# Performance work log

Hardware: AMD Instinct MI355X
Metric: run time of the kernel (lower is better)

The kernel has to match this reference:

```python
import jax, jax.numpy as jnp
import numpy as np

E = 1_000_000
C_IN = 11
H = 64
N_LAYERS = 4
LN_EPS = 1e-5


def setup_inputs() -> dict:
    key = jax.random.key(0)
    ks = jax.random.split(key, 12)
    x = jax.random.normal(ks[0], (E, C_IN), dtype=jnp.float32)
    neighbors = jax.random.randint(ks[1], (E, 4), 0, E)
    s0 = 1.0 / np.sqrt(5 * C_IN)
    s1 = 1.0 / np.sqrt(5 * H)
    w0 = jax.random.uniform(ks[2], (5 * C_IN, H), jnp.float32, -s0, s0)
    b0 = jax.random.uniform(ks[3], (H,), jnp.float32, -s0, s0)
    w_rest = jax.random.uniform(ks[4], (N_LAYERS - 1, 5 * H, H), jnp.float32, -s1, s1)
    b_rest = jax.random.uniform(ks[5], (N_LAYERS - 1, H), jnp.float32, -s1, s1)
    ln_g = jnp.ones((N_LAYERS, H), jnp.float32)
    ln_b = jnp.zeros((N_LAYERS, H), jnp.float32)
    sc1 = 1.0 / np.sqrt(H)
    sc2 = 1.0 / np.sqrt(H // 2)
    cw1 = jax.random.uniform(ks[6], (H, H // 2), jnp.float32, -sc1, sc1)
    cb1 = jax.random.uniform(ks[7], (H // 2,), jnp.float32, -sc1, sc1)
    cw2 = jax.random.uniform(ks[8], (H // 2, 1), jnp.float32, -sc2, sc2)
    cb2 = jax.random.uniform(ks[9], (1,), jnp.float32, -sc2, sc2)
    return {"x": x, "neighbors": neighbors, "w0": w0, "b0": b0,
            "w_rest": w_rest, "b_rest": b_rest, "ln_g": ln_g, "ln_b": ln_b,
            "cw1": cw1, "cb1": cb1, "cw2": cw2, "cb2": cb2}


def _mesh_conv(x, neighbors, W, b):
    # Gather 4-ring neighbor features: [E,4,C]
    n = x[neighbors]
    a, bb, c, d = n[:, 0], n[:, 1], n[:, 2], n[:, 3]
    # Symmetric MeshCNN features -> 5*C, then linear projection.
    feats = jnp.concatenate([x, jnp.abs(a - c), a + c, jnp.abs(bb - d), bb + d], axis=-1)
    return feats @ W + b


def _layernorm(h, g, b):
    mu = jnp.mean(h, axis=-1, keepdims=True)
    var = jnp.var(h, axis=-1, keepdims=True)
    return (h - mu) * jax.lax.rsqrt(var + LN_EPS) * g + b


def reference(x, neighbors, w0, b0, w_rest, b_rest, ln_g, ln_b, cw1, cb1, cw2, cb2):
    # Layer 0 (no residual; dropout is identity in eval mode)
    h = jax.nn.relu(_layernorm(_mesh_conv(x, neighbors, w0, b0), ln_g[0], ln_b[0]))
    x = h
    for i in range(1, N_LAYERS):
        h = _mesh_conv(x, neighbors, w_rest[i - 1], b_rest[i - 1])
        h = jax.nn.relu(_layernorm(h, ln_g[i], ln_b[i]))
        x = h + x  # residual from layer 2 onward (shapes match)
    z = jax.nn.relu(x @ cw1 + cb1)
    logits = (z @ cw2 + cb2).squeeze(-1)
    return logits
```

## Files before the change

kernel.cpp:

```cpp
#include <hip/hip_runtime.h>
#include <hip/hip_bf16.h>
#include <math.h>

#define E_EDGES 1000000
#define LN_EPS  1e-5f

typedef unsigned short u16;
typedef __bf16 bf16x8 __attribute__((ext_vector_type(8)));
typedef float  f32x16 __attribute__((ext_vector_type(16)));

__device__ __forceinline__ float lo2f(unsigned d) {
    union { unsigned u; float f; } v; v.u = d << 16; return v.f;
}
__device__ __forceinline__ float hi2f(unsigned d) {
    union { unsigned u; float f; } v; v.u = d & 0xffff0000u; return v.f;
}
__device__ __forceinline__ float bf2f(u16 u) {
    union { unsigned u; float f; } v; v.u = ((unsigned)u) << 16; return v.f;
}
__device__ __forceinline__ unsigned pk2(float lo, float hi) {
    __hip_bfloat162 h = __float22bfloat162_rn(make_float2(lo, hi));
    unsigned r; __builtin_memcpy(&r, &h, 4); return r;
}

__global__ __launch_bounds__(256) void wconv_kernel(
    const float* __restrict__ wr, const float* __restrict__ w0,
    const float* __restrict__ cw1, u16* __restrict__ wf)
{
    const int s = blockIdx.x * 256 + threadIdx.x;
    if (s >= 8448) return;
    const int l    = s & 63;
    const int half = l >> 5;
    uint4 pk;
    if (s < 3 * 2560) {
        const int col = ((s >> 6) & 1) * 32 + (l & 31);
        const int L  = s / 2560;
        const int sl = s % 2560;
        const int kb = (sl >> 7) * 16 + half * 8;
        const float* W = wr + L * 320 * 64;
        pk.x = pk2(W[(kb+0)*64+col], W[(kb+1)*64+col]);
        pk.y = pk2(W[(kb+2)*64+col], W[(kb+3)*64+col]);
        pk.z = pk2(W[(kb+4)*64+col], W[(kb+5)*64+col]);
        pk.w = pk2(W[(kb+6)*64+col], W[(kb+7)*64+col]);
    } else if (s < 8192) {
        const int col = ((s >> 6) & 1) * 32 + (l & 31);
        const int sl = s - 3 * 2560;
        const int kb = (sl >> 7) * 16 + half * 8;
        float v[8];
        #pragma unroll
        for (int p = 0; p < 8; ++p) v[p] = (kb + p < 55) ? w0[(kb+p)*64 + col] : 0.f;
        pk.x = pk2(v[0],v[1]); pk.y = pk2(v[2],v[3]);
        pk.z = pk2(v[4],v[5]); pk.w = pk2(v[6],v[7]);
    } else {
        const int sl = s - 8192;
        const int ks = sl >> 6;
        const int col = l & 31;
        const int kb = ks * 16 + half * 8;
        pk.x = pk2(cw1[(kb+0)*32+col], cw1[(kb+1)*32+col]);
        pk.y = pk2(cw1[(kb+2)*32+col], cw1[(kb+3)*32+col]);
        pk.z = pk2(cw1[(kb+4)*32+col], cw1[(kb+5)*32+col]);
        pk.w = pk2(cw1[(kb+6)*32+col], cw1[(kb+7)*32+col]);
    }
    *(uint4*)&wf[(size_t)s * 8] = pk;
}

__global__ __launch_bounds__(256) void xprep_kernel(
    const float* __restrict__ x, u16* __restrict__ xc)
{
    __shared__ float xs[2816];
    const int t = threadIdx.x;
    const long long i0 = (long long)blockIdx.x * 704;
    #pragma unroll
    for (int k = 0; k < 3; ++k) {
        const int idx = t + k * 256;
        if (idx < 704 && i0 + idx < 2750000)
            *(float4*)&xs[idx * 4] = ((const float4*)x)[i0 + idx];
    }
    __syncthreads();
    const size_t e = (size_t)blockIdx.x * 256 + t;
    if (e < E_EDGES) {
        const float* r = &xs[t * 11];
        uint4 o0, o1;
        o0.x = pk2(r[0], r[1]);  o0.y = pk2(r[2], r[3]);
        o0.z = pk2(r[4], r[5]);  o0.w = pk2(r[6], r[7]);
        o1.x = pk2(r[8], r[9]);  o1.y = pk2(r[10], 0.f);
        o1.z = 0u;               o1.w = 0u;
        *(uint4*)&xc[e * 16]     = o0;
        *(uint4*)&xc[e * 16 + 8] = o1;
    }
}

__global__ __launch_bounds__(128, 4) void layer0_mfma(
    const u16* __restrict__ xc, const int* __restrict__ nbr,
    const u16* __restrict__ wf0, const float* __restrict__ bias,
    const float* __restrict__ lng, const float* __restrict__ lnb,
    u16* __restrict__ xout)
{
    __shared__ u16 sm[4608];
    u16* afrag = sm;
    u16* raw   = sm + 2048;
    const int t  = threadIdx.x;
    const int l  = t & 63;
    const int wv = t >> 6;
    const int e0 = blockIdx.x * 32;
    const int el = t >> 2, cq = t & 3;

    {
        const size_t e = (size_t)(e0 + el);
        const int4 n = *(const int4*)(nbr + 4 * e);
        const int nj = (cq == 0) ? n.x : (cq == 1) ? n.y : (cq == 2) ? n.z : n.w;
        const u16* nr = xc + (size_t)nj * 16;
        u16* dst = raw + (el * 5 + 1 + cq) * 16;
        *(uint4*)dst       = *(const uint4*)nr;
        *(uint4*)(dst + 8) = *(const uint4*)(nr + 8);
        if (cq == 0) {
            const u16* xr = xc + e * 16;
            u16* od = raw + (el * 5) * 16;
            *(uint4*)od       = *(const uint4*)xr;
            *(uint4*)(od + 8) = *(const uint4*)(xr + 8);
        }
    }
    __syncthreads();

    {
        const u16* R = raw + el * 80;
        float f[16];
        if (cq == 0) {
            #pragma unroll
            for (int i = 0; i < 11; ++i) f[i] = bf2f(R[i]);
            #pragma unroll
            for (int i = 0; i < 5; ++i) f[11+i] = fabsf(bf2f(R[16+i]) - bf2f(R[48+i]));
        } else if (cq == 1) {
            #pragma unroll
            for (int i = 0; i < 6; ++i) f[i] = fabsf(bf2f(R[16+5+i]) - bf2f(R[48+5+i]));
            #pragma unroll
            for (int i = 0; i < 10; ++i) f[6+i] = bf2f(R[16+i]) + bf2f(R[48+i]);
        } else if (cq == 2) {
            f[0] = bf2f(R[16+10]) + bf2f(R[48+10]);
            #pragma unroll
            for (int i = 0; i < 11; ++i) f[1+i] = fabsf(bf2f(R[32+i]) - bf2f(R[64+i]));
            #pragma unroll
            for (int i = 0; i < 4; ++i) f[12+i] = bf2f(R[32+i]) + bf2f(R[64+i]);
        } else {
            #pragma unroll
            for (int i = 0; i < 7; ++i) f[i] = bf2f(R[32+4+i]) + bf2f(R[64+4+i]);
            #pragma unroll
            for (int i = 7; i < 16; ++i) f[i] = 0.f;
        }
        #pragma unroll
        for (int hh = 0; hh < 2; ++hh) {
            uint4 pk;
            pk.x = pk2(f[hh*8+0], f[hh*8+1]);
            pk.y = pk2(f[hh*8+2], f[hh*8+3]);
            pk.z = pk2(f[hh*8+4], f[hh*8+5]);
            pk.w = pk2(f[hh*8+6], f[hh*8+7]);
            const int gsw = (el + 32 * hh) ^ cq;
            *(uint4*)(afrag + (size_t)(cq * 64 + gsw) * 8) = pk;
        }
    }
    __syncthreads();

    const int nt = wv;
    f32x16 acc = {};
    const u16* bb = wf0 + (size_t)(nt * 64 + l) * 8;
    #pragma unroll
    for (int ks = 0; ks < 4; ++ks) {
        const bf16x8 a8 = *(const bf16x8*)(afrag + (size_t)(ks * 64 + (l ^ ks)) * 8);
        const bf16x8 b8 = *(const bf16x8*)(bb + ks * 1024);
        acc = __builtin_amdgcn_mfma_f32_32x32x16_bf16(a8, b8, acc, 0, 0, 0);
    }
    __syncthreads();

    float* ebuf = (float*)sm;
    {
        const int col  = nt * 32 + (l & 31);
        const int quad = l >> 5;
        const float bc = bias[col];
        #pragma unroll
        for (int r = 0; r < 16; ++r) {
            const int row = (r & 3) + 8 * (r >> 2) + 4 * quad;
            ebuf[row * 68 + col] = acc[r] + bc;
        }
    }
    __syncthreads();

    {
        const float* rp = ebuf + el * 68 + cq * 16;
        float v[16];
        float s = 0.f, qs = 0.f;
        #pragma unroll
        for (int i = 0; i < 16; ++i) { v[i] = rp[i]; s += v[i]; qs += v[i] * v[i]; }
        s  += __shfl_xor(s, 1);  s  += __shfl_xor(s, 2);
        qs += __shfl_xor(qs, 1); qs += __shfl_xor(qs, 2);
        const float mu   = s * (1.f / 64.f);
        const float var  = qs * (1.f / 64.f) - mu * mu;
        const float rinv = rsqrtf(var + LN_EPS);
        const size_t e   = (size_t)(e0 + el);
        u16* outp        = xout + e * 64 + cq * 16;
        #pragma unroll
        for (int h = 0; h < 2; ++h) {
            uint4 o; unsigned* op = (unsigned*)&o;
            #pragma unroll
            for (int i = 0; i < 4; ++i) {
                const int ci = cq * 16 + h * 8 + i * 2;
                const float y0 = fmaxf(fmaf((v[h*8+i*2]   - mu) * rinv, lng[ci],   lnb[ci]),   0.f);
                const float y1 = fmaxf(fmaf((v[h*8+i*2+1] - mu) * rinv, lng[ci+1], lnb[ci+1]), 0.f);
                op[i] = pk2(y0, y1);
            }
            *(uint4*)(outp + h * 8) = o;
        }
    }
}

__device__ __forceinline__ void feat_pair(
    const uint4 u, const uint4 w, uint4& gd, uint4& gs)
{
    const unsigned* up = (const unsigned*)&u;
    const unsigned* wp = (const unsigned*)&w;
    unsigned* dp = (unsigned*)&gd;
    unsigned* sp = (unsigned*)&gs;
    #pragma unroll
    for (int i = 0; i < 4; ++i) {
        const float u0 = lo2f(up[i]), u1 = hi2f(up[i]);
        const float w0 = lo2f(wp[i]), w1 = hi2f(wp[i]);
        dp[i] = pk2(u0 - w0, u1 - w1) & 0x7FFF7FFFu;
        sp[i] = pk2(u0 + w0, u1 + w1);
    }
}

__global__ __launch_bounds__(128, 4) void layer_mfma(
    const u16* __restrict__ xin, const int* __restrict__ nbr,
    const u16* __restrict__ wf, const float* __restrict__ bias,
    const float* __restrict__ lng, const float* __restrict__ lnb,
    u16* __restrict__ xout)
{
    __shared__ u16 afrag[12 * 64 * 8];
    const int t  = threadIdx.x;
    const int l  = t & 63;
    const int wv = t >> 6;
    const int e0 = blockIdx.x * 32;
    const int el = t >> 2;
    const int cq = t & 3;
    const int nt = wv;

    const size_t e = (size_t)(e0 + el);
    const int4 n = *(const int4*)(nbr + 4 * e);
    const u16* xr = xin + e * 64           + cq * 16;
    const u16* ar = xin + (size_t)n.x * 64 + cq * 16;
    const u16* br = xin + (size_t)n.y * 64 + cq * 16;
    const u16* cr = xin + (size_t)n.z * 64 + cq * 16;
    const u16* dr = xin + (size_t)n.w * 64 + cq * 16;
    const uint4 xv0 = *(const uint4*)(xr);     const uint4 xv1 = *(const uint4*)(xr + 8);
    const uint4 av0 = *(const uint4*)(ar);     const uint4 av1 = *(const uint4*)(ar + 8);
    const uint4 bv0 = *(const uint4*)(br);     const uint4 bv1 = *(const uint4*)(br + 8);
    const uint4 cv0 = *(const uint4*)(cr);     const uint4 cv1 = *(const uint4*)(cr + 8);
    const uint4 dv0 = *(const uint4*)(dr);     const uint4 dv1 = *(const uint4*)(dr + 8);

    {
        #pragma unroll
        for (int w8 = 0; w8 < 2; ++w8) {
            const int gsw = (el + 32 * w8) ^ cq;
            uint4 g1, g2;
            feat_pair(w8 ? av1 : av0, w8 ? cv1 : cv0, g1, g2);
            *(uint4*)(afrag + (size_t)(((0*4 + cq) * 64) + gsw) * 8) = w8 ? xv1 : xv0;
            *(uint4*)(afrag + (size_t)(((1*4 + cq) * 64) + gsw) * 8) = g1;
            *(uint4*)(afrag + (size_t)(((2*4 + cq) * 64) + gsw) * 8) = g2;
        }
    }
    __syncthreads();

    f32x16 acc = {};
    const u16* bb = wf + (size_t)(nt * 64 + l) * 8;
    #pragma unroll
    for (int ks = 0; ks < 12; ++ks) {
        const bf16x8 a8 = *(const bf16x8*)(afrag + (size_t)(ks * 64 + (l ^ (ks & 3))) * 8);
        const bf16x8 b8 = *(const bf16x8*)(bb + ks * 1024);
        acc = __builtin_amdgcn_mfma_f32_32x32x16_bf16(a8, b8, acc, 0, 0, 0);
    }
    __syncthreads();

    {
        #pragma unroll
        for (int w8 = 0; w8 < 2; ++w8) {
            const int gsw = (el + 32 * w8) ^ cq;
            uint4 g3, g4;
            feat_pair(w8 ? bv1 : bv0, w8 ? dv1 : dv0, g3, g4);
            *(uint4*)(afrag + (size_t)(((0*4 + cq) * 64) + gsw) * 8) = g3;
            *(uint4*)(afrag + (size_t)(((1*4 + cq) * 64) + gsw) * 8) = g4;
        }
    }
    __syncthreads();

    #pragma unroll
    for (int ks = 0; ks < 8; ++ks) {
        const bf16x8 a8 = *(const bf16x8*)(afrag + (size_t)(ks * 64 + (l ^ (ks & 3))) * 8);
        const bf16x8 b8 = *(const bf16x8*)(bb + (12 + ks) * 1024);
        acc = __builtin_amdgcn_mfma_f32_32x32x16_bf16(a8, b8, acc, 0, 0, 0);
    }
    __syncthreads();

    float* ebuf = (float*)afrag;
    {
        const int col  = nt * 32 + (l & 31);
        const int quad = l >> 5;
        const float bc = bias[col];
        #pragma unroll
        for (int r = 0; r < 16; ++r) {
            const int row = (r & 3) + 8 * (r >> 2) + 4 * quad;
            ebuf[row * 68 + col] = acc[r] + bc;
        }
    }
    __syncthreads();

    {
        float lgv[16], lbv[16];
        #pragma unroll
        for (int j = 0; j < 4; ++j) {
            *(float4*)&lgv[j * 4] = *(const float4*)(lng + cq * 16 + j * 4);
            *(float4*)&lbv[j * 4] = *(const float4*)(lnb + cq * 16 + j * 4);
        }
        const float* rp = ebuf + el * 68 + cq * 16;
        float v[16];
        float s = 0.f, qs = 0.f;
        #pragma unroll
        for (int i = 0; i < 16; ++i) { v[i] = rp[i]; s += v[i]; qs += v[i] * v[i]; }
        s  += __shfl_xor(s, 1);  s  += __shfl_xor(s, 2);
        qs += __shfl_xor(qs, 1); qs += __shfl_xor(qs, 2);
        const float mu   = s * (1.f / 64.f);
        const float var  = qs * (1.f / 64.f) - mu * mu;
        const float rinv = rsqrtf(var + LN_EPS);
        u16* outp        = xout + e * 64 + cq * 16;
        #pragma unroll
        for (int h = 0; h < 2; ++h) {
            const uint4 res = h ? xv1 : xv0;
            const unsigned* rr = (const unsigned*)&res;
            uint4 o; unsigned* op = (unsigned*)&o;
            #pragma unroll
            for (int i = 0; i < 4; ++i) {
                const int k = h * 8 + i * 2;
                const float y0 = fmaxf(fmaf((v[k]   - mu) * rinv, lgv[k],   lbv[k]),   0.f) + lo2f(rr[i]);
                const float y1 = fmaxf(fmaf((v[k+1] - mu) * rinv, lgv[k+1], lbv[k+1]), 0.f) + hi2f(rr[i]);
                op[i] = pk2(y0, y1);
            }
            *(uint4*)(outp + h * 8) = o;
        }
    }
}

__global__ __launch_bounds__(128, 4) void layer_head_mfma(
    const u16* __restrict__ xin, const int* __restrict__ nbr,
    const u16* __restrict__ wf, const float* __restrict__ bias,
    const float* __restrict__ lng, const float* __restrict__ lnb,
    const u16* __restrict__ wfh, const float* __restrict__ cb1,
    const float* __restrict__ cw2, const float* __restrict__ cb2,
    float* __restrict__ out)
{
    __shared__ u16 lds[8192];
    u16*   afrag = lds;
    u16*   ybuf  = lds + 6144;
    float* hbuf2 = (float*)lds;
    const int t  = threadIdx.x;
    const int l  = t & 63;
    const int wv = t >> 6;
    const int e0 = blockIdx.x * 32;
    const int el = t >> 2;
    const int cq = t & 3;
    const int nt = wv;

    const size_t e = (size_t)(e0 + el);
    const int4 n = *(const int4*)(nbr + 4 * e);
    const u16* xr = xin + e * 64           + cq * 16;
    const u16* ar = xin + (size_t)n.x * 64 + cq * 16;
    const u16* br = xin + (size_t)n.y * 64 + cq * 16;
    const u16* cr = xin + (size_t)n.z * 64 + cq * 16;
    const u16* dr = xin + (size_t)n.w * 64 + cq * 16;
    const uint4 xv0 = *(const uint4*)(xr);     const uint4 xv1 = *(const uint4*)(xr + 8);
    const uint4 av0 = *(const uint4*)(ar);     const uint4 av1 = *(const uint4*)(ar + 8);
    const uint4 bv0 = *(const uint4*)(br);     const uint4 bv1 = *(const uint4*)(br + 8);
    const uint4 cv0 = *(const uint4*)(cr);     const uint4 cv1 = *(const uint4*)(cr + 8);
    const uint4 dv0 = *(const uint4*)(dr);     const uint4 dv1 = *(const uint4*)(dr + 8);

    {
        #pragma unroll
        for (int w8 = 0; w8 < 2; ++w8) {
            const int gsw = (el + 32 * w8) ^ cq;
            uint4 g1, g2;
            feat_pair(w8 ? av1 : av0, w8 ? cv1 : cv0, g1, g2);
            *(uint4*)(afrag + (size_t)(((0*4 + cq) * 64) + gsw) * 8) = w8 ? xv1 : xv0;
            *(uint4*)(afrag + (size_t)(((1*4 + cq) * 64) + gsw) * 8) = g1;
            *(uint4*)(afrag + (size_t)(((2*4 + cq) * 64) + gsw) * 8) = g2;
        }
    }
    __syncthreads();

    f32x16 acc = {};
    const u16* bb = wf + (size_t)(nt * 64 + l) * 8;
    #pragma unroll
    for (int ks = 0; ks < 12; ++ks) {
        const bf16x8 a8 = *(const bf16x8*)(afrag + (size_t)(ks * 64 + (l ^ (ks & 3))) * 8);
        const bf16x8 b8 = *(const bf16x8*)(bb + ks * 1024);
        acc = __builtin_amdgcn_mfma_f32_32x32x16_bf16(a8, b8, acc, 0, 0, 0);
    }
    __syncthreads();

    {
        #pragma unroll
        for (int w8 = 0; w8 < 2; ++w8) {
            const int gsw = (el + 32 * w8) ^ cq;
            uint4 g3, g4;
            feat_pair(w8 ? bv1 : bv0, w8 ? dv1 : dv0, g3, g4);
            *(uint4*)(afrag + (size_t)(((0*4 + cq) * 64) + gsw) * 8) = g3;
            *(uint4*)(afrag + (size_t)(((1*4 + cq) * 64) + gsw) * 8) = g4;
        }
    }
    __syncthreads();

    #pragma unroll
    for (int ks = 0; ks < 8; ++ks) {
        const bf16x8 a8 = *(const bf16x8*)(afrag + (size_t)(ks * 64 + (l ^ (ks & 3))) * 8);
        const bf16x8 b8 = *(const bf16x8*)(bb + (12 + ks) * 1024);
        acc = __builtin_amdgcn_mfma_f32_32x32x16_bf16(a8, b8, acc, 0, 0, 0);
    }
    __syncthreads();

    float* ebuf = (float*)afrag;
    {
        const int col  = nt * 32 + (l & 31);
        const int quad = l >> 5;
        const float bc = bias[col];
        #pragma unroll
        for (int r = 0; r < 16; ++r) {
            const int row = (r & 3) + 8 * (r >> 2) + 4 * quad;
            ebuf[row * 68 + col] = acc[r] + bc;
        }
    }
    __syncthreads();

    {
        float lgv[16], lbv[16];
        #pragma unroll
        for (int j = 0; j < 4; ++j) {
            *(float4*)&lgv[j * 4] = *(const float4*)(lng + cq * 16 + j * 4);
            *(float4*)&lbv[j * 4] = *(const float4*)(lnb + cq * 16 + j * 4);
        }
        const float* rp = ebuf + el * 68 + cq * 16;
        float v[16];
        float s = 0.f, qs = 0.f;
        #pragma unroll
        for (int i = 0; i < 16; ++i) { v[i] = rp[i]; s += v[i]; qs += v[i] * v[i]; }
        s  += __shfl_xor(s, 1);  s  += __shfl_xor(s, 2);
        qs += __shfl_xor(qs, 1); qs += __shfl_xor(qs, 2);
        const float mu   = s * (1.f / 64.f);
        const float var  = qs * (1.f / 64.f) - mu * mu;
        const float rinv = rsqrtf(var + LN_EPS);
        #pragma unroll
        for (int h = 0; h < 2; ++h) {
            const uint4 res = h ? xv1 : xv0;
            const unsigned* rr = (const unsigned*)&res;
            uint4 o; unsigned* op = (unsigned*)&o;
            #pragma unroll
            for (int i = 0; i < 4; ++i) {
                const int k = h * 8 + i * 2;
                const float y0 = fmaxf(fmaf((v[k]   - mu) * rinv, lgv[k],   lbv[k]),   0.f) + lo2f(rr[i]);
                const float y1 = fmaxf(fmaf((v[k+1] - mu) * rinv, lgv[k+1], lbv[k+1]), 0.f) + hi2f(rr[i]);
                op[i] = pk2(y0, y1);
            }
            const int gsw = (el + 32 * h) ^ cq;
            *(uint4*)(ybuf + (size_t)((cq * 64) + gsw) * 8) = o;
        }
    }
    __syncthreads();

    if (wv == 0) {
        f32x16 a2 = {};
        #pragma unroll
        for (int ks = 0; ks < 4; ++ks) {
            const bf16x8 a8 = *(const bf16x8*)(ybuf + (size_t)((ks * 64) + (l ^ ks)) * 8);
            const bf16x8 b8 = *(const bf16x8*)(wfh + (size_t)(ks * 64 + l) * 8);
            a2 = __builtin_amdgcn_mfma_f32_32x32x16_bf16(a8, b8, a2, 0, 0, 0);
        }
        const int col = l & 31;
        const float bc1 = cb1[col];
        const float w2v = cw2[col];
        #pragma unroll
        for (int r = 0; r < 16; ++r) {
            const int row = (r & 3) + 8 * (r >> 2) + 4 * (l >> 5);
            hbuf2[row * 33 + col] = fmaxf(a2[r] + bc1, 0.f) * w2v;
        }
    }
    __syncthreads();

    if (t < 64) {
        const int edge = t >> 1, part = t & 1;
        const float* rp = hbuf2 + edge * 33 + part * 16;
        float s = 0.f;
        #pragma unroll
        for (int i = 0; i < 16; ++i) s += rp[i];
        s += __shfl_xor(s, 1);
        if (part == 0) out[e0 + edge] = s + cb2[0];
    }
}

__global__ __launch_bounds__(256) void head_mfma(
    const u16* __restrict__ xin,
    const float* __restrict__ cw1, const float* __restrict__ cb1,
    const float* __restrict__ cw2, const float* __restrict__ cb2,
    float* __restrict__ out)
{
    __shared__ float hbuf[4][32 * 33];
    const int t    = threadIdx.x;
    const int l    = t & 63;
    const int wv   = t >> 6;
    const int col  = l & 31;
    const int half = l >> 5;

    bf16x8 bf[4];
    #pragma unroll
    for (int ks = 0; ks < 4; ++ks) {
        const int kb = ks * 16 + half * 8;
        uint4 pk;
        pk.x = pk2(cw1[(kb+0)*32 + col], cw1[(kb+1)*32 + col]);
        pk.y = pk2(cw1[(kb+2)*32 + col], cw1[(kb+3)*32 + col]);
        pk.z = pk2(cw1[(kb+4)*32 + col], cw1[(kb+5)*32 + col]);
        pk.w = pk2(cw1[(kb+6)*32 + col], cw1[(kb+7)*32 + col]);
        __builtin_memcpy(&bf[ks], &pk, 16);
    }
    const float bc = cb1[col];
    const float w2 = cw2[col];
    const float b2 = cb2[0];

    int tile = blockIdx.x * 4 + wv;
    const int valid = tile < (E_EDGES / 32);
    if (!valid) tile = E_EDGES / 32 - 1;
    const size_t e0 = (size_t)tile * 32;
    const u16* xb = xin + (e0 + col) * 64 + half * 8;
    f32x16 acc = {};
    #pragma unroll
    for (int ks = 0; ks < 4; ++ks) {
        const bf16x8 a8 = *(const bf16x8*)(xb + ks * 16);
        acc = __builtin_amdgcn_mfma_f32_32x32x16_bf16(a8, bf[ks], acc, 0, 0, 0);
    }
    float* hb = hbuf[wv];
    #pragma unroll
    for (int r = 0; r < 16; ++r) {
        const int row = (r & 3) + 8 * (r >> 2) + 4 * half;
        hb[row * 33 + col] = fmaxf(acc[r] + bc, 0.f) * w2;
    }
    __syncthreads();
    const int row2 = l >> 1, part = l & 1;
    const float* rp = hb + row2 * 33 + part * 16;
    float s = 0.f;
    #pragma unroll
    for (int i = 0; i < 16; ++i) s += rp[i];
    s += __shfl_xor(s, 1);
    if (valid && part == 0) out[e0 + row2] = s + b2;
}

extern "C" void kernel_launch(void* const* d_in, const int* in_sizes, int n_in,
                              void* d_out, int out_size, void* d_ws, size_t ws_size,
                              hipStream_t stream)
{
    (void)in_sizes; (void)n_in; (void)out_size;
    const float* x   = (const float*)d_in[0];
    const int*   nbr = (const int*)d_in[1];
    const float* w0  = (const float*)d_in[2];
    const float* b0  = (const float*)d_in[3];
    const float* wr  = (const float*)d_in[4];
    const float* br  = (const float*)d_in[5];
    const float* lg  = (const float*)d_in[6];
    const float* lb  = (const float*)d_in[7];
    const float* cw1 = (const float*)d_in[8];
    const float* cb1 = (const float*)d_in[9];
    const float* cw2 = (const float*)d_in[10];
    const float* cb2 = (const float*)d_in[11];
    float* out = (float*)d_out;

    u16* xa = (u16*)d_ws;
    u16* xb = xa + (size_t)E_EDGES * 64;
    u16* xc = xb;

    const size_t act_bytes = 2ull * E_EDGES * 64 * 2;
    const size_t wf_bytes  = 8448ull * 16;
    const bool fused = (ws_size >= act_bytes + wf_bytes);
    u16* wfrag = fused ? (u16*)((char*)d_ws + act_bytes) : (u16*)d_out;

    const dim3 blk128(128);
    wconv_kernel<<<dim3(33), dim3(256), 0, stream>>>(wr, w0, cw1, wfrag);
    xprep_kernel<<<dim3((E_EDGES + 255) / 256), dim3(256), 0, stream>>>(x, xc);
    layer0_mfma<<<dim3(E_EDGES / 32), blk128, 0, stream>>>(xc, nbr, wfrag + 3*20480, b0, lg, lb, xa);
    layer_mfma<<<dim3(E_EDGES / 32), blk128, 0, stream>>>(xa, nbr, wfrag,         br,       lg + 64,  lb + 64,  xb);
    layer_mfma<<<dim3(E_EDGES / 32), blk128, 0, stream>>>(xb, nbr, wfrag + 20480, br + 64,  lg + 128, lb + 128, xa);
    if (fused) {
        layer_head_mfma<<<dim3(E_EDGES / 32), blk128, 0, stream>>>(
            xa, nbr, wfrag + 40960, br + 128, lg + 192, lb + 192,
            wfrag + 65536, cb1, cw2, cb2, out);
    } else {
        layer_mfma<<<dim3(E_EDGES / 32), blk128, 0, stream>>>(xa, nbr, wfrag + 40960,
            br + 128, lg + 192, lb + 192, xb);
        head_mfma<<<dim3((E_EDGES / 32 + 3) / 4), dim3(256), 0, stream>>>(xb, cw1, cb1, cw2, cb2, out);
    }
}
```

Before: 591.5 us.

## Process two edge tiles per block with register-resident weights and prefetched gathers

Each block of layer_mfma and layer_head_mfma now handles 64 edges as two 32-edge tiles. It keeps all 20 weight fragments (plus the head fragments) in registers, loaded once per block instead of once per tile. The neighbor-row gathers for the second tile are issued right after the first tile's pack, so their latency overlaps the first tile's MFMA and layernorm work. Barriers become explicit lgkmcnt waits with scheduling fences, and the LN gamma/beta are held packed as bf16. The cost is much higher register use (launch bounds no longer request 4 blocks per CU), a separate ebuf in LDS that raises shared-memory use, and half as many blocks, which can lower occupancy.

```diff
diff --git a/kernel.cpp b/kernel.cpp
--- a/kernel.cpp
+++ b/kernel.cpp
@@ -8,6 +8,13 @@
 typedef unsigned short u16;
 typedef __bf16 bf16x8 __attribute__((ext_vector_type(8)));
 typedef float  f32x16 __attribute__((ext_vector_type(16)));
+
+#define BAR_LGKM() do {                                       \
+    __builtin_amdgcn_sched_barrier(0);                        \
+    asm volatile("s_waitcnt lgkmcnt(0)" ::: "memory");        \
+    __builtin_amdgcn_s_barrier();                             \
+    __builtin_amdgcn_sched_barrier(0);                        \
+} while (0)
 
 __device__ __forceinline__ float lo2f(unsigned d) {
     union { unsigned u; float f; } v; v.u = d << 16; return v.f;
@@ -212,6 +219,23 @@
     }
 }
 
+struct GRows { uint4 x0,x1,a0,a1,b0,b1,c0,c1,d0,d1; };
+
+__device__ __forceinline__ void rows_issue(
+    const u16* __restrict__ xin, const int4 n, size_t e, int cq, GRows& R)
+{
+    const u16* xr = xin + e * 64           + cq * 16;
+    const u16* ar = xin + (size_t)n.x * 64 + cq * 16;
+    const u16* br = xin + (size_t)n.y * 64 + cq * 16;
+    const u16* cr = xin + (size_t)n.z * 64 + cq * 16;
+    const u16* dr = xin + (size_t)n.w * 64 + cq * 16;
+    R.x0 = *(const uint4*)xr;  R.x1 = *(const uint4*)(xr + 8);
+    R.a0 = *(const uint4*)ar;  R.a1 = *(const uint4*)(ar + 8);
+    R.b0 = *(const uint4*)br;  R.b1 = *(const uint4*)(br + 8);
+    R.c0 = *(const uint4*)cr;  R.c1 = *(const uint4*)(cr + 8);
+    R.d0 = *(const uint4*)dr;  R.d1 = *(const uint4*)(dr + 8);
+}
+
 __device__ __forceinline__ void feat_pair(
     const uint4 u, const uint4 w, uint4& gd, uint4& gs)
 {
@@ -228,126 +252,143 @@
     }
 }
 
-__global__ __launch_bounds__(128, 4) void layer_mfma(
+__device__ __forceinline__ void pack_c1(
+    u16* __restrict__ afrag, int el, int cq, const GRows& R)
+{
+    #pragma unroll
+    for (int w8 = 0; w8 < 2; ++w8) {
+        const int gsw = (el + 32 * w8) ^ cq;
+        uint4 g1, g2;
+        feat_pair(w8 ? R.a1 : R.a0, w8 ? R.c1 : R.c0, g1, g2);
+        *(uint4*)(afrag + (size_t)(((0*4 + cq) * 64) + gsw) * 8) = w8 ? R.x1 : R.x0;
+        *(uint4*)(afrag + (size_t)(((1*4 + cq) * 64) + gsw) * 8) = g1;
+        *(uint4*)(afrag + (size_t)(((2*4 + cq) * 64) + gsw) * 8) = g2;
+    }
+}
+
+__device__ __forceinline__ void pack_c2(
+    u16* __restrict__ afrag, int el, int cq, const GRows& R)
+{
+    #pragma unroll
+    for (int w8 = 0; w8 < 2; ++w8) {
+        const int gsw = (el + 32 * w8) ^ cq;
+        uint4 g3, g4;
+        feat_pair(w8 ? R.b1 : R.b0, w8 ? R.d1 : R.d0, g3, g4);
+        *(uint4*)(afrag + (size_t)(((0*4 + cq) * 64) + gsw) * 8) = g3;
+        *(uint4*)(afrag + (size_t)(((1*4 + cq) * 64) + gsw) * 8) = g4;
+    }
+}
+
+__global__ __launch_bounds__(128) void layer_mfma(
     const u16* __restrict__ xin, const int* __restrict__ nbr,
     const u16* __restrict__ wf, const float* __restrict__ bias,
     const float* __restrict__ lng, const float* __restrict__ lnb,
     u16* __restrict__ xout)
 {
-    __shared__ u16 afrag[12 * 64 * 8];
+    __shared__ u16   afrag[12 * 64 * 8];
+    __shared__ float ebuf[32 * 68];
     const int t  = threadIdx.x;
     const int l  = t & 63;
-    const int wv = t >> 6;
-    const int e0 = blockIdx.x * 32;
+    const int nt = t >> 6;
+    const int e0 = blockIdx.x * 64;
     const int el = t >> 2;
     const int cq = t & 3;
-    const int nt = wv;
-
-    const size_t e = (size_t)(e0 + el);
-    const int4 n = *(const int4*)(nbr + 4 * e);
-    const u16* xr = xin + e * 64           + cq * 16;
-    const u16* ar = xin + (size_t)n.x * 64 + cq * 16;
-    const u16* br = xin + (size_t)n.y * 64 + cq * 16;
-    const u16* cr = xin + (size_t)n.z * 64 + cq * 16;
-    const u16* dr = xin + (size_t)n.w * 64 + cq * 16;
-    const uint4 xv0 = *(const uint4*)(xr);     const uint4 xv1 = *(const uint4*)(xr + 8);
-    const uint4 av0 = *(const uint4*)(ar);     const uint4 av1 = *(const uint4*)(ar + 8);
-    const uint4 bv0 = *(const uint4*)(br);     const uint4 bv1 = *(const uint4*)(br + 8);
-    const uint4 cv0 = *(const uint4*)(cr);     const uint4 cv1 = *(const uint4*)(cr + 8);
-    const uint4 dv0 = *(const uint4*)(dr);     const uint4 dv1 = *(const uint4*)(dr + 8);
-
-    {
-        #pragma unroll
-        for (int w8 = 0; w8 < 2; ++w8) {
-            const int gsw = (el + 32 * w8) ^ cq;
-            uint4 g1, g2;
-            feat_pair(w8 ? av1 : av0, w8 ? cv1 : cv0, g1, g2);
-            *(uint4*)(afrag + (size_t)(((0*4 + cq) * 64) + gsw) * 8) = w8 ? xv1 : xv0;
-            *(uint4*)(afrag + (size_t)(((1*4 + cq) * 64) + gsw) * 8) = g1;
-            *(uint4*)(afrag + (size_t)(((2*4 + cq) * 64) + gsw) * 8) = g2;
-        }
-    }
-    __syncthreads();
-
-    f32x16 acc = {};
-    const u16* bb = wf + (size_t)(nt * 64 + l) * 8;
-    #pragma unroll
-    for (int ks = 0; ks < 12; ++ks) {
-        const bf16x8 a8 = *(const bf16x8*)(afrag + (size_t)(ks * 64 + (l ^ (ks & 3))) * 8);
-        const bf16x8 b8 = *(const bf16x8*)(bb + ks * 1024);
-        acc = __builtin_amdgcn_mfma_f32_32x32x16_bf16(a8, b8, acc, 0, 0, 0);
-    }
-    __syncthreads();
-
-    {
-        #pragma unroll
-        for (int w8 = 0; w8 < 2; ++w8) {
-            const int gsw = (el + 32 * w8) ^ cq;
-            uint4 g3, g4;
-            feat_pair(w8 ? bv1 : bv0, w8 ? dv1 : dv0, g3, g4);
-            *(uint4*)(afrag + (size_t)(((0*4 + cq) * 64) + gsw) * 8) = g3;
-            *(uint4*)(afrag + (size_t)(((1*4 + cq) * 64) + gsw) * 8) = g4;
-        }
-    }
-    __syncthreads();
-
-    #pragma unroll
-    for (int ks = 0; ks < 8; ++ks) {
-        const bf16x8 a8 = *(const bf16x8*)(afrag + (size_t)(ks * 64 + (l ^ (ks & 3))) * 8);
-        const bf16x8 b8 = *(const bf16x8*)(bb + (12 + ks) * 1024);
-        acc = __builtin_amdgcn_mfma_f32_32x32x16_bf16(a8, b8, acc, 0, 0, 0);
-    }
-    __syncthreads();
-
-    float* ebuf = (float*)afrag;
-    {
-        const int col  = nt * 32 + (l & 31);
-        const int quad = l >> 5;
-        const float bc = bias[col];
-        #pragma unroll
-        for (int r = 0; r < 16; ++r) {
-            const int row = (r & 3) + 8 * (r >> 2) + 4 * quad;
-            ebuf[row * 68 + col] = acc[r] + bc;
-        }
-    }
-    __syncthreads();
-
-    {
-        float lgv[16], lbv[16];
-        #pragma unroll
-        for (int j = 0; j < 4; ++j) {
-            *(float4*)&lgv[j * 4] = *(const float4*)(lng + cq * 16 + j * 4);
-            *(float4*)&lbv[j * 4] = *(const float4*)(lnb + cq * 16 + j * 4);
-        }
-        const float* rp = ebuf + el * 68 + cq * 16;
-        float v[16];
-        float s = 0.f, qs = 0.f;
-        #pragma unroll
-        for (int i = 0; i < 16; ++i) { v[i] = rp[i]; s += v[i]; qs += v[i] * v[i]; }
-        s  += __shfl_xor(s, 1);  s  += __shfl_xor(s, 2);
-        qs += __shfl_xor(qs, 1); qs += __shfl_xor(qs, 2);
-        const float mu   = s * (1.f / 64.f);
-        const float var  = qs * (1.f / 64.f) - mu * mu;
-        const float rinv = rsqrtf(var + LN_EPS);
-        u16* outp        = xout + e * 64 + cq * 16;
-        #pragma unroll
-        for (int h = 0; h < 2; ++h) {
-            const uint4 res = h ? xv1 : xv0;
-            const unsigned* rr = (const unsigned*)&res;
-            uint4 o; unsigned* op = (unsigned*)&o;
-            #pragma unroll
-            for (int i = 0; i < 4; ++i) {
-                const int k = h * 8 + i * 2;
-                const float y0 = fmaxf(fmaf((v[k]   - mu) * rinv, lgv[k],   lbv[k]),   0.f) + lo2f(rr[i]);
-                const float y1 = fmaxf(fmaf((v[k+1] - mu) * rinv, lgv[k+1], lbv[k+1]), 0.f) + hi2f(rr[i]);
-                op[i] = pk2(y0, y1);
+
+    unsigned lgpk[8], lbpk[8];
+    #pragma unroll
+    for (int j = 0; j < 4; ++j) {
+        const float4 g4 = *(const float4*)(lng + cq * 16 + j * 4);
+        const float4 b4 = *(const float4*)(lnb + cq * 16 + j * 4);
+        lgpk[j*2] = pk2(g4.x, g4.y); lgpk[j*2+1] = pk2(g4.z, g4.w);
+        lbpk[j*2] = pk2(b4.x, b4.y); lbpk[j*2+1] = pk2(b4.z, b4.w);
+    }
+    const int colc = nt * 32 + (l & 31);
+    const float bc = bias[colc];
+    bf16x8 breg[20];
+    {
+        const u16* bb = wf + (size_t)(nt * 64 + l) * 8;
+        #pragma unroll
+        for (int ks = 0; ks < 20; ++ks) breg[ks] = *(const bf16x8*)(bb + ks * 1024);
+    }
+
+    GRows cur, nxt;
+    const int4 n1 = *(const int4*)(nbr + 4 * (size_t)(e0 + 32 + el));
+    {
+        const int4 n0 = *(const int4*)(nbr + 4 * (size_t)(e0 + el));
+        rows_issue(xin, n0, (size_t)(e0 + el), cq, cur);
+    }
+
+    #pragma unroll
+    for (int tt = 0; tt < 2; ++tt) {
+        const int eb = e0 + tt * 32;
+        pack_c1(afrag, el, cq, cur);
+        BAR_LGKM();
+
+        if (tt == 0)
+            rows_issue(xin, n1, (size_t)(e0 + 32 + el), cq, nxt);
+
+        f32x16 acc = {};
+        #pragma unroll
+        for (int ks = 0; ks < 12; ++ks) {
+            const bf16x8 a8 = *(const bf16x8*)(afrag + (size_t)(ks * 64 + (l ^ (ks & 3))) * 8);
+            acc = __builtin_amdgcn_mfma_f32_32x32x16_bf16(a8, breg[ks], acc, 0, 0, 0);
+        }
+        BAR_LGKM();
+
+        pack_c2(afrag, el, cq, cur);
+        BAR_LGKM();
+
+        #pragma unroll
+        for (int ks = 0; ks < 8; ++ks) {
+            const bf16x8 a8 = *(const bf16x8*)(afrag + (size_t)(ks * 64 + (l ^ (ks & 3))) * 8);
+            acc = __builtin_amdgcn_mfma_f32_32x32x16_bf16(a8, breg[12 + ks], acc, 0, 0, 0);
+        }
+
+        {
+            const int quad = l >> 5;
+            #pragma unroll
+            for (int r = 0; r < 16; ++r) {
+                const int row = (r & 3) + 8 * (r >> 2) + 4 * quad;
+                ebuf[row * 68 + colc] = acc[r] + bc;
             }
-            *(uint4*)(outp + h * 8) = o;
-        }
-    }
-}
-
-__global__ __launch_bounds__(128, 4) void layer_head_mfma(
+        }
+        BAR_LGKM();
+
+        {
+            const float* rp = ebuf + el * 68 + cq * 16;
+            float v[16];
+            float s = 0.f, qs = 0.f;
+            #pragma unroll
+            for (int i = 0; i < 16; ++i) { v[i] = rp[i]; s += v[i]; qs += v[i] * v[i]; }
+            s  += __shfl_xor(s, 1);  s  += __shfl_xor(s, 2);
+            qs += __shfl_xor(qs, 1); qs += __shfl_xor(qs, 2);
+            const float mu   = s * (1.f / 64.f);
+            const float var  = qs * (1.f / 64.f) - mu * mu;
+            const float rinv = rsqrtf(var + LN_EPS);
+            u16* outp = xout + (size_t)(eb + el) * 64 + cq * 16;
+            #pragma unroll
+            for (int h = 0; h < 2; ++h) {
+                const uint4 res = h ? cur.x1 : cur.x0;
+                const unsigned* rr = (const unsigned*)&res;
+                uint4 o; unsigned* op = (unsigned*)&o;
+                #pragma unroll
+                for (int i = 0; i < 4; ++i) {
+                    const int k = h * 8 + i * 2;
+                    const int j = h * 4 + i;
+                    const float y0 = fmaxf(fmaf((v[k]   - mu) * rinv, lo2f(lgpk[j]), lo2f(lbpk[j])), 0.f) + lo2f(rr[i]);
+                    const float y1 = fmaxf(fmaf((v[k+1] - mu) * rinv, hi2f(lgpk[j]), hi2f(lbpk[j])), 0.f) + hi2f(rr[i]);
+                    op[i] = pk2(y0, y1);
+                }
+                *(uint4*)(outp + h * 8) = o;
+            }
+        }
+        BAR_LGKM();
+
+        cur = nxt;
+    }
+}
+
+__global__ __launch_bounds__(128) void layer_head_mfma(
     const u16* __restrict__ xin, const int* __restrict__ nbr,
     const u16* __restrict__ wf, const float* __restrict__ bias,
     const float* __restrict__ lng, const float* __restrict__ lnb,
@@ -355,149 +396,142 @@
     const float* __restrict__ cw2, const float* __restrict__ cb2,
     float* __restrict__ out)
 {
-    __shared__ u16 lds[8192];
-    u16*   afrag = lds;
-    u16*   ybuf  = lds + 6144;
-    float* hbuf2 = (float*)lds;
+    __shared__ u16   afrag[12 * 64 * 8];
+    __shared__ float ebuf[32 * 68];
+    __shared__ u16   ybuf[4 * 64 * 8];
+    float* hbuf2 = (float*)afrag;
     const int t  = threadIdx.x;
     const int l  = t & 63;
-    const int wv = t >> 6;
-    const int e0 = blockIdx.x * 32;
+    const int nt = t >> 6;
+    const int e0 = blockIdx.x * 64;
     const int el = t >> 2;
     const int cq = t & 3;
-    const int nt = wv;
-
-    const size_t e = (size_t)(e0 + el);
-    const int4 n = *(const int4*)(nbr + 4 * e);
-    const u16* xr = xin + e * 64           + cq * 16;
-    const u16* ar = xin + (size_t)n.x * 64 + cq * 16;
-    const u16* br = xin + (size_t)n.y * 64 + cq * 16;
-    const u16* cr = xin + (size_t)n.z * 64 + cq * 16;
-    const u16* dr = xin + (size_t)n.w * 64 + cq * 16;
-    const uint4 xv0 = *(const uint4*)(xr);     const uint4 xv1 = *(const uint4*)(xr + 8);
-    const uint4 av0 = *(const uint4*)(ar);     const uint4 av1 = *(const uint4*)(ar + 8);
-    const uint4 bv0 = *(const uint4*)(br);     const uint4 bv1 = *(const uint4*)(br + 8);
-    const uint4 cv0 = *(const uint4*)(cr);     const uint4 cv1 = *(const uint4*)(cr + 8);
-    const uint4 dv0 = *(const uint4*)(dr);     const uint4 dv1 = *(const uint4*)(dr + 8);
-
-    {
-        #pragma unroll
-        for (int w8 = 0; w8 < 2; ++w8) {
-            const int gsw = (el + 32 * w8) ^ cq;
-            uint4 g1, g2;
-            feat_pair(w8 ? av1 : av0, w8 ? cv1 : cv0, g1, g2);
-            *(uint4*)(afrag + (size_t)(((0*4 + cq) * 64) + gsw) * 8) = w8 ? xv1 : xv0;
-            *(uint4*)(afrag + (size_t)(((1*4 + cq) * 64) + gsw) * 8) = g1;
-            *(uint4*)(afrag + (size_t)(((2*4 + cq) * 64) + gsw) * 8) = g2;
-        }
-    }
-    __syncthreads();
-
-    f32x16 acc = {};
-    const u16* bb = wf + (size_t)(nt * 64 + l) * 8;
-    #pragma unroll
-    for (int ks = 0; ks < 12; ++ks) {
-        const bf16x8 a8 = *(const bf16x8*)(afrag + (size_t)(ks * 64 + (l ^ (ks & 3))) * 8);
-        const bf16x8 b8 = *(const bf16x8*)(bb + ks * 1024);
-        acc = __builtin_amdgcn_mfma_f32_32x32x16_bf16(a8, b8, acc, 0, 0, 0);
-    }
-    __syncthreads();
-
-    {
-        #pragma unroll
-        for (int w8 = 0; w8 < 2; ++w8) {
-            const int gsw = (el + 32 * w8) ^ cq;
-            uint4 g3, g4;
-            feat_pair(w8 ? bv1 : bv0, w8 ? dv1 : dv0, g3, g4);
-            *(uint4*)(afrag + (size_t)(((0*4 + cq) * 64) + gsw) * 8) = g3;
-            *(uint4*)(afrag + (size_t)(((1*4 + cq) * 64) + gsw) * 8) = g4;
-        }
-    }
-    __syncthreads();
-
-    #pragma unroll
-    for (int ks = 0; ks < 8; ++ks) {
-        const bf16x8 a8 = *(const bf16x8*)(afrag + (size_t)(ks * 64 + (l ^ (ks & 3))) * 8);
-        const bf16x8 b8 = *(const bf16x8*)(bb + (12 + ks) * 1024);
-        acc = __builtin_amdgcn_mfma_f32_32x32x16_bf16(a8, b8, acc, 0, 0, 0);
-    }
-    __syncthreads();
-
-    float* ebuf = (float*)afrag;
-    {
-        const int col  = nt * 32 + (l & 31);
-        const int quad = l >> 5;
-        const float bc = bias[col];
-        #pragma unroll
-        for (int r = 0; r < 16; ++r) {
-            const int row = (r & 3) + 8 * (r >> 2) + 4 * quad;
-            ebuf[row * 68 + col] = acc[r] + bc;
-        }
-    }
-    __syncthreads();
-
-    {
-        float lgv[16], lbv[16];
-        #pragma unroll
-        for (int j = 0; j < 4; ++j) {
-            *(float4*)&lgv[j * 4] = *(const float4*)(lng + cq * 16 + j * 4);
-            *(float4*)&lbv[j * 4] = *(const float4*)(lnb + cq * 16 + j * 4);
-        }
-        const float* rp = ebuf + el * 68 + cq * 16;
-        float v[16];
-        float s = 0.f, qs = 0.f;
-        #pragma unroll
-        for (int i = 0; i < 16; ++i) { v[i] = rp[i]; s += v[i]; qs += v[i] * v[i]; }
-        s  += __shfl_xor(s, 1);  s  += __shfl_xor(s, 2);
-        qs += __shfl_xor(qs, 1); qs += __shfl_xor(qs, 2);
-        const float mu   = s * (1.f / 64.f);
-        const float var  = qs * (1.f / 64.f) - mu * mu;
-        const float rinv = rsqrtf(var + LN_EPS);
-        #pragma unroll
-        for (int h = 0; h < 2; ++h) {
-            const uint4 res = h ? xv1 : xv0;
-            const unsigned* rr = (const unsigned*)&res;
-            uint4 o; unsigned* op = (unsigned*)&o;
-            #pragma unroll
-            for (int i = 0; i < 4; ++i) {
-                const int k = h * 8 + i * 2;
-                const float y0 = fmaxf(fmaf((v[k]   - mu) * rinv, lgv[k],   lbv[k]),   0.f) + lo2f(rr[i]);
-                const float y1 = fmaxf(fmaf((v[k+1] - mu) * rinv, lgv[k+1], lbv[k+1]), 0.f) + hi2f(rr[i]);
-                op[i] = pk2(y0, y1);
+
+    unsigned lgpk[8], lbpk[8];
+    #pragma unroll
+    for (int j = 0; j < 4; ++j) {
+        const float4 g4 = *(const float4*)(lng + cq * 16 + j * 4);
+        const float4 b4 = *(const float4*)(lnb + cq * 16 + j * 4);
+        lgpk[j*2] = pk2(g4.x, g4.y); lgpk[j*2+1] = pk2(g4.z, g4.w);
+        lbpk[j*2] = pk2(b4.x, b4.y); lbpk[j*2+1] = pk2(b4.z, b4.w);
+    }
+    const int colc = nt * 32 + (l & 31);
+    const float bc = bias[colc];
+    bf16x8 breg[20];
+    {
+        const u16* bb = wf + (size_t)(nt * 64 + l) * 8;
+        #pragma unroll
+        for (int ks = 0; ks < 20; ++ks) breg[ks] = *(const bf16x8*)(bb + ks * 1024);
+    }
+    const int colh = l & 31;
+    const float bc1 = cb1[colh];
+    const float w2v = cw2[colh];
+    const float b2v = cb2[0];
+    bf16x8 bfh[4];
+    #pragma unroll
+    for (int ks = 0; ks < 4; ++ks)
+        bfh[ks] = *(const bf16x8*)(wfh + (size_t)(ks * 64 + l) * 8);
+
+    GRows cur, nxt;
+    const int4 n1 = *(const int4*)(nbr + 4 * (size_t)(e0 + 32 + el));
+    {
+        const int4 n0 = *(const int4*)(nbr + 4 * (size_t)(e0 + el));
+        rows_issue(xin, n0, (size_t)(e0 + el), cq, cur);
+    }
+
+    #pragma unroll
+    for (int tt = 0; tt < 2; ++tt) {
+        const int eb = e0 + tt * 32;
+        pack_c1(afrag, el, cq, cur);
+        BAR_LGKM();
+
+        if (tt == 0)
+            rows_issue(xin, n1, (size_t)(e0 + 32 + el), cq, nxt);
+
+        f32x16 acc = {};
+        #pragma unroll
+        for (int ks = 0; ks < 12; ++ks) {
+            const bf16x8 a8 = *(const bf16x8*)(afrag + (size_t)(ks * 64 + (l ^ (ks & 3))) * 8);
+            acc = __builtin_amdgcn_mfma_f32_32x32x16_bf16(a8, breg[ks], acc, 0, 0, 0);
+        }
+        BAR_LGKM();
+
+        pack_c2(afrag, el, cq, cur);
+        BAR_LGKM();
+
+        #pragma unroll
+        for (int ks = 0; ks < 8; ++ks) {
+            const bf16x8 a8 = *(const bf16x8*)(afrag + (size_t)(ks * 64 + (l ^ (ks & 3))) * 8);
+            acc = __builtin_amdgcn_mfma_f32_32x32x16_bf16(a8, breg[12 + ks], acc, 0, 0, 0);
+        }
+
+        {
+            const int quad = l >> 5;
+            #pragma unroll
+            for (int r = 0; r < 16; ++r) {
+                const int row = (r & 3) + 8 * (r >> 2) + 4 * quad;
+                ebuf[row * 68 + colc] = acc[r] + bc;
             }
-            const int gsw = (el + 32 * h) ^ cq;
-            *(uint4*)(ybuf + (size_t)((cq * 64) + gsw) * 8) = o;
-        }
-    }
-    __syncthreads();
-
-    if (wv == 0) {
-        f32x16 a2 = {};
-        #pragma unroll
-        for (int ks = 0; ks < 4; ++ks) {
-            const bf16x8 a8 = *(const bf16x8*)(ybuf + (size_t)((ks * 64) + (l ^ ks)) * 8);
-            const bf16x8 b8 = *(const bf16x8*)(wfh + (size_t)(ks * 64 + l) * 8);
-            a2 = __builtin_amdgcn_mfma_f32_32x32x16_bf16(a8, b8, a2, 0, 0, 0);
-        }
-        const int col = l & 31;
-        const float bc1 = cb1[col];
-        const float w2v = cw2[col];
-        #pragma unroll
-        for (int r = 0; r < 16; ++r) {
-            const int row = (r & 3) + 8 * (r >> 2) + 4 * (l >> 5);
-            hbuf2[row * 33 + col] = fmaxf(a2[r] + bc1, 0.f) * w2v;
-        }
-    }
-    __syncthreads();
-
-    if (t < 64) {
-        const int edge = t >> 1, part = t & 1;
-        const float* rp = hbuf2 + edge * 33 + part * 16;
-        float s = 0.f;
-        #pragma unroll
-        for (int i = 0; i < 16; ++i) s += rp[i];
-        s += __shfl_xor(s, 1);
-        if (part == 0) out[e0 + edge] = s + cb2[0];
+        }
+        BAR_LGKM();
+
+        {
+            const float* rp = ebuf + el * 68 + cq * 16;
+            float v[16];
+            float s = 0.f, qs = 0.f;
+            #pragma unroll
+            for (int i = 0; i < 16; ++i) { v[i] = rp[i]; s += v[i]; qs += v[i] * v[i]; }
+            s  += __shfl_xor(s, 1);  s  += __shfl_xor(s, 2);
+            qs += __shfl_xor(qs, 1); qs += __shfl_xor(qs, 2);
+            const float mu   = s * (1.f / 64.f);
+            const float var  = qs * (1.f / 64.f) - mu * mu;
+            const float rinv = rsqrtf(var + LN_EPS);
+            #pragma unroll
+            for (int h = 0; h < 2; ++h) {
+                const uint4 res = h ? cur.x1 : cur.x0;
+                const unsigned* rr = (const unsigned*)&res;
+                uint4 o; unsigned* op = (unsigned*)&o;
+                #pragma unroll
+                for (int i = 0; i < 4; ++i) {
+                    const int k = h * 8 + i * 2;
+                    const int j = h * 4 + i;
+                    const float y0 = fmaxf(fmaf((v[k]   - mu) * rinv, lo2f(lgpk[j]), lo2f(lbpk[j])), 0.f) + lo2f(rr[i]);
+                    const float y1 = fmaxf(fmaf((v[k+1] - mu) * rinv, hi2f(lgpk[j]), hi2f(lbpk[j])), 0.f) + hi2f(rr[i]);
+                    op[i] = pk2(y0, y1);
+                }
+                const int gsw = (el + 32 * h) ^ cq;
+                *(uint4*)(ybuf + (size_t)((cq * 64) + gsw) * 8) = o;
+            }
+        }
+        BAR_LGKM();
+
+        if (nt == 0) {
+            f32x16 a2 = {};
+            #pragma unroll
+            for (int ks = 0; ks < 4; ++ks) {
+                const bf16x8 a8 = *(const bf16x8*)(ybuf + (size_t)((ks * 64) + (l ^ ks)) * 8);
+                a2 = __builtin_amdgcn_mfma_f32_32x32x16_bf16(a8, bfh[ks], a2, 0, 0, 0);
+            }
+            #pragma unroll
+            for (int r = 0; r < 16; ++r) {
+                const int row = (r & 3) + 8 * (r >> 2) + 4 * (l >> 5);
+                hbuf2[row * 33 + colh] = fmaxf(a2[r] + bc1, 0.f) * w2v;
+            }
+        }
+        BAR_LGKM();
+
+        if (t < 64) {
+            const int edge = t >> 1, part = t & 1;
+            const float* rp = hbuf2 + edge * 33 + part * 16;
+            float s = 0.f;
+            #pragma unroll
+            for (int i = 0; i < 16; ++i) s += rp[i];
+            s += __shfl_xor(s, 1);
+            if (part == 0) out[eb + edge] = s + b2v;
+        }
+        BAR_LGKM();
+
+        cur = nxt;
     }
 }
 
@@ -588,14 +622,14 @@
     wconv_kernel<<<dim3(33), dim3(256), 0, stream>>>(wr, w0, cw1, wfrag);
     xprep_kernel<<<dim3((E_EDGES + 255) / 256), dim3(256), 0, stream>>>(x, xc);
     layer0_mfma<<<dim3(E_EDGES / 32), blk128, 0, stream>>>(xc, nbr, wfrag + 3*20480, b0, lg, lb, xa);
-    layer_mfma<<<dim3(E_EDGES / 32), blk128, 0, stream>>>(xa, nbr, wfrag,         br,       lg + 64,  lb + 64,  xb);
-    layer_mfma<<<dim3(E_EDGES / 32), blk128, 0, stream>>>(xb, nbr, wfrag + 20480, br + 64,  lg + 128, lb + 128, xa);
+    layer_mfma<<<dim3(E_EDGES / 64), blk128, 0, stream>>>(xa, nbr, wfrag,         br,       lg + 64,  lb + 64,  xb);
+    layer_mfma<<<dim3(E_EDGES / 64), blk128, 0, stream>>>(xb, nbr, wfrag + 20480, br + 64,  lg + 128, lb + 128, xa);
     if (fused) {
-        layer_head_mfma<<<dim3(E_EDGES / 32), blk128, 0, stream>>>(
+        layer_head_mfma<<<dim3(E_EDGES / 64), blk128, 0, stream>>>(
             xa, nbr, wfrag + 40960, br + 128, lg + 192, lb + 192,
             wfrag + 65536, cb1, cw2, cb2, out);
     } else {
-        layer_mfma<<<dim3(E_EDGES / 32), blk128, 0, stream>>>(xa, nbr, wfrag + 40960,
+        layer_mfma<<<dim3(E_EDGES / 64), blk128, 0, stream>>>(xa, nbr, wfrag + 40960,
             br + 128, lg + 192, lb + 192, xb);
         head_mfma<<<dim3((E_EDGES / 32 + 3) / 4), dim3(256), 0, stream>>>(xb, cw1, cb1, cw2, cb2, out);
     }
```

After: 756.9 us. +28.0%, slower.
